# Optimization experiments

Measured on AMD Instinct MI355X. Metric: run time of the kernel, lower is better.

## Reference

```python
import jax, jax.numpy as jnp
import numpy as np

N = 100000   # nodes
F = 128      # feature dim (== numEdges ctor arg)
H = 64       # hidden_dim
E = 1600000  # edges (avg degree 16)


def setup_inputs() -> dict:
    key = jax.random.key(0)
    ks = jax.random.split(key, 8)
    x = jax.random.normal(ks[0], (N, F), dtype=jnp.float32)
    edge_index = jax.random.randint(ks[1], (2, E), 0, N)
    sF = 1.0 / np.sqrt(F)
    sH = 1.0 / np.sqrt(H)
    conv_W = jax.random.normal(ks[2], (F, F), dtype=jnp.float32) * sF  # GCNConv linear weight
    conv_b = jnp.zeros((F,), dtype=jnp.float32)
    w1 = jax.random.normal(ks[3], (H, F), dtype=jnp.float32) * sF
    b1 = jnp.zeros((H,), dtype=jnp.float32)
    w2 = jax.random.normal(ks[4], (H, H), dtype=jnp.float32) * sH
    b2 = jnp.zeros((H,), dtype=jnp.float32)
    w3 = jax.random.normal(ks[5], (1, H), dtype=jnp.float32) * sH
    b3 = jnp.zeros((1,), dtype=jnp.float32)
    return dict(x=x, edge_index=edge_index, conv_W=conv_W, conv_b=conv_b,
                w1=w1, b1=b1, w2=w2, b2=b2, w3=w3, b3=b3)


def reference(x, edge_index, conv_W, conv_b, w1, b1, w2, b2, w3, b3):
    n = x.shape[0]
    # --- GCNConv: D^{-1/2}(A+I)D^{-1/2} X W + b ---
    xw = x @ conv_W.T                                   # [N, F]
    loops = jnp.arange(n)
    src = jnp.concatenate([edge_index[0], loops])       # add self-loops
    dst = jnp.concatenate([edge_index[1], loops])
    deg = jax.ops.segment_sum(jnp.ones(src.shape[0], xw.dtype), dst, num_segments=n)
    dinv = jnp.where(deg > 0, jax.lax.rsqrt(deg), 0.0)
    norm = dinv[src] * dinv[dst]                        # [E+N]
    h = jax.ops.segment_sum(xw[src] * norm[:, None], dst, num_segments=n) + conv_b  # [N, F]
    # --- MedianAggregation (index=None -> single segment, 'lower' interpolation) ---
    med = jnp.sort(h, axis=0)[(n - 1) // 2][None, :]    # [1, F]
    # --- tanh MLP ---
    a = jnp.tanh(med @ w1.T + b1)
    a = jnp.tanh(a @ w2.T + b2)
    return a @ w3.T + b3                                # [1, 1]
```

## Files before the change

kernel.cpp:

```cpp
#include <hip/hip_runtime.h>
#include <math.h>


#define CAP    24576
#define CCAP   96
#define DSTR   32
#define OVCAP  4096
#define SPCAP  2048
#define BCAP   4608
#define NBKMAX 400
#define CH     4096

typedef __attribute__((ext_vector_type(8))) short short8;
typedef __attribute__((ext_vector_type(4))) float f32x4;
typedef __attribute__((ext_vector_type(8))) _Float16 half8;
typedef __attribute__((ext_vector_type(2))) _Float16 half2v;

__device__ __forceinline__ unsigned ordKey(float x) {
    unsigned u = __float_as_uint(x);
    return (u & 0x80000000u) ? ~u : (u | 0x80000000u);
}
__device__ __forceinline__ float keyToFloat(unsigned k) {
    unsigned bits = (k & 0x80000000u) ? (k & 0x7FFFFFFFu) : ~k;
    return __uint_as_float(bits);
}
__device__ __forceinline__ unsigned short f2bf(float f) {
    unsigned u = __float_as_uint(f);
    return (unsigned short)((u + 0x7FFFu + ((u >> 16) & 1u)) >> 16);
}

__global__ void k_init(int* __restrict__ cursor, int* __restrict__ below,
                       int* __restrict__ candCnt, int* __restrict__ ovCnt,
                       const float* __restrict__ W, short* __restrict__ Whi,
                       short* __restrict__ Wlo, int nbk) {
    if (blockIdx.x == 1) {
        for (int idx = threadIdx.x; idx < 16384; idx += 256) {
            int j = idx & 7, lane = (idx >> 3) & 63;
            int t = (idx >> 9) & 7, s = idx >> 12;
            int row = t * 16 + (lane & 15);
            int k = s * 32 + (lane >> 4) * 8 + j;
            float w = W[row * 128 + k];
            unsigned short hb = f2bf(w);
            float hf = __uint_as_float((unsigned)hb << 16);
            Whi[idx] = (short)hb;
            Wlo[idx] = (short)f2bf(w - hf);
        }
        return;
    }
    int t = threadIdx.x;
    for (int i = t; i < nbk; i += 256) cursor[i] = 0;
    if (t < 128) { below[t] = 0; candCnt[t] = 0; }
    if (t == 0) { ovCnt[0] = 0; ovCnt[1] = 0; }
}

__global__ __launch_bounds__(256) void k_binGemm(
        const float* __restrict__ x, const short* __restrict__ Whi,
        const short* __restrict__ Wlo, _Float16* __restrict__ xw, int n, int GB,
        const int* __restrict__ src, const int* __restrict__ dst, int E,
        int* __restrict__ cursor, int2* __restrict__ binned,
        int* __restrict__ ovCnt, int2* __restrict__ ovBuf, int nbk) {
    __shared__ char smem[39168];
    const int t = threadIdx.x;
    if ((int)blockIdx.x < GB) {
        float* trn = (float*)smem;
        const int lane = t & 63, wv = t >> 6;
        const int quad = lane >> 4, m = lane & 15;
        const int rowBase = blockIdx.x * 64 + wv * 16;
        const int r = rowBase + m;
        const int rl = r < n ? r : (n - 1);
        f32x4 acc[8];
        #pragma unroll
        for (int q = 0; q < 8; q++) acc[q] = (f32x4){0.f, 0.f, 0.f, 0.f};
        #pragma unroll
        for (int s = 0; s < 4; s++) {
            const float* xp = x + (size_t)rl * 128 + s * 32 + quad * 8;
            float4 p0 = *(const float4*)xp;
            float4 p1 = *(const float4*)(xp + 4);
            float f[8] = {p0.x, p0.y, p0.z, p0.w, p1.x, p1.y, p1.z, p1.w};
            short8 ah, al;
            #pragma unroll
            for (int j = 0; j < 8; j++) {
                unsigned short hb = f2bf(f[j]);
                float hf = __uint_as_float((unsigned)hb << 16);
                ah[j] = (short)hb;
                al[j] = (short)f2bf(f[j] - hf);
            }
            #pragma unroll
            for (int q = 0; q < 8; q++) {
                short8 bh = *(const short8*)(Whi + (((s * 8 + q) * 64 + lane) << 3));
                short8 bl = *(const short8*)(Wlo + (((s * 8 + q) * 64 + lane) << 3));
                acc[q] = __builtin_amdgcn_mfma_f32_16x16x32_bf16(ah, bh, acc[q], 0, 0, 0);
                acc[q] = __builtin_amdgcn_mfma_f32_16x16x32_bf16(al, bh, acc[q], 0, 0, 0);
                acc[q] = __builtin_amdgcn_mfma_f32_16x16x32_bf16(ah, bl, acc[q], 0, 0, 0);
            }
        }
        float* tw = trn + wv * (16 * 132);
        #pragma unroll
        for (int q = 0; q < 8; q++)
            #pragma unroll
            for (int e = 0; e < 4; e++)
                tw[(quad * 4 + e) * 132 + q * 16 + m] = acc[q][e];
        #pragma unroll
        for (int i = 0; i < 4; i++) {
            int row = i * 4 + (lane >> 4);
            int c8 = lane & 15;
            const float* tp = tw + row * 132 + c8 * 8;
            float4 p0 = *(const float4*)tp;
            float4 p1 = *(const float4*)(tp + 4);
            half8 o;
            o[0] = (_Float16)p0.x; o[1] = (_Float16)p0.y;
            o[2] = (_Float16)p0.z; o[3] = (_Float16)p0.w;
            o[4] = (_Float16)p1.x; o[5] = (_Float16)p1.y;
            o[6] = (_Float16)p1.z; o[7] = (_Float16)p1.w;
            int grow = rowBase + row;
            if (grow < n) *(half8*)(xw + (size_t)grow * 128 + c8 * 8) = o;
        }
    } else {
        int2* stage = (int2*)smem;
        int* hist  = (int*)(smem + 32768);
        int* gbase = hist + NBKMAX;
        int* hist2 = gbase + NBKMAX;
        int* sbase = hist2 + NBKMAX;
        const int e0 = ((int)blockIdx.x - GB) * CH;
        const int len = min(CH, E - e0);
        for (int i = t; i < nbk; i += 256) { hist[i] = 0; hist2[i] = 0; }
        __syncthreads();
        for (int k = t; k < len; k += 256) {
            int s = src[e0 + k], d = dst[e0 + k];
            stage[k] = make_int2(s, d);
            atomicAdd(&hist[d >> 8], 1);
        }
        __syncthreads();
        for (int i = t; i < nbk; i += 256) {
            int c = hist[i];
            if (c) {
                int g = atomicAdd(&cursor[i], c);
                if (g + c <= BCAP) gbase[i] = g;
                else {
                    gbase[i] = -1;
                    sbase[i] = atomicAdd(ovCnt, c);
                }
            }
        }
        __syncthreads();
        for (int k = t; k < len; k += 256) {
            int2 e = stage[k];
            int b = e.y >> 8;
            int p = atomicAdd(&hist2[b], 1);
            int g = gbase[b];
            if (g >= 0) binned[(size_t)b * BCAP + g + p] = e;
            else {
                int o = sbase[b] + p;
                if (o < OVCAP) ovBuf[o] = make_int2(e.y, e.x);
            }
        }
    }
}

__global__ __launch_bounds__(256) void k_build(int2* __restrict__ binned,
                                               const int* __restrict__ cursor,
                                               float* __restrict__ dinv,
                                               unsigned char* __restrict__ deg8,
                                               int* __restrict__ ovCnt,
                                               int2* __restrict__ ovBuf,
                                               int* __restrict__ spillNodes, int n) {
    __shared__ int ladj[256 * DSTR];
    __shared__ int lcnt[256];
    const int b = blockIdx.x, t = threadIdx.x;
    const int cnt = min(cursor[b], BCAP);
    const size_t e0 = (size_t)b * BCAP;
    lcnt[t] = 0;
    __syncthreads();
    for (int k = t; k < cnt; k += 256) {
        int2 e = binned[e0 + k];
        int li = e.y & 255;
        int pos = atomicAdd(&lcnt[li], 1);
        if (pos < DSTR) ladj[li * DSTR + pos] = e.x;
        else {
            int o = atomicAdd(ovCnt, 1);
            if (o < OVCAP) ovBuf[o] = make_int2(e.y, e.x);
        }
    }
    __syncthreads();
    int4* adjOut = (int4*)((int*)binned + e0 * 2);
    const int4* lsrc4 = (const int4*)ladj;
    for (int i = t; i < 2048; i += 256) adjOut[i] = lsrc4[i];
    int node = b * 256 + t;
    if (node < n) {
        int deg = lcnt[t];
        dinv[node] = (float)(1.0 / sqrt((double)(deg + 1)));
        deg8[node] = (unsigned char)(deg < 255 ? deg : 255);
        if (deg > DSTR) {
            int p = atomicAdd(ovCnt + 1, 1);
            if (p < SPCAP) spillNodes[p] = node;
        }
    }
}

__global__ __launch_bounds__(256) void k_aggS(const _Float16* __restrict__ xw,
                                              const unsigned char* __restrict__ deg8,
                                              const int* __restrict__ adjAll,
                                              const float* __restrict__ dinv,
                                              const float* __restrict__ conv_b,
                                              float* __restrict__ hS, int n, int ns) {
    const int si = blockIdx.x * 4 + (threadIdx.x >> 6);
    if (si >= ns) return;
    const int d = si << 5;
    const int lane = threadIdx.x & 63;
    const int l32 = lane & 31;
    int degT = deg8[d];
    const int degB = degT < DSTR ? degT : DSTR;
    const float dd = dinv[d];
    const int* adjRow = adjAll + (size_t)(d >> 8) * (BCAP * 2) + (d & 255) * DSTR;
    int aj = adjRow[l32];
    bool ev = (lane < 32) && (l32 < degB);
    int ajs = ev ? aj : 0;
    float dv = ev ? dinv[ajs] : 0.f;
    const half2v* xwv = (const half2v*)xw;
    half2v a = xwv[(size_t)d * 64 + lane];
    float ax = dd * dd * (float)a.x, ay = dd * dd * (float)a.y;
    int j = 0;
    for (; j + 8 <= degB; j += 8) {
        int s[8];
        float w[8];
        #pragma unroll
        for (int q = 0; q < 8; q++) {
            s[q] = __shfl(ajs, j + q, 64);
            w[q] = dd * __shfl(dv, j + q, 64);
        }
        #pragma unroll
        for (int q = 0; q < 8; q++) {
            half2v v = xwv[(size_t)s[q] * 64 + lane];
            ax += w[q] * (float)v.x;
            ay += w[q] * (float)v.y;
        }
    }
    if (j < degB) {
        int s[8];
        float w[8];
        #pragma unroll
        for (int q = 0; q < 8; q++) {
            int idx = j + q;
            bool ok = idx < degB;
            int lsrc = ok ? idx : 0;
            int sv = __shfl(ajs, lsrc, 64);
            float wv = dd * __shfl(dv, lsrc, 64);
            s[q] = ok ? sv : 0;
            w[q] = ok ? wv : 0.f;
        }
        #pragma unroll
        for (int q = 0; q < 8; q++) {
            half2v v = xwv[(size_t)s[q] * 64 + lane];
            ax += w[q] * (float)v.x;
            ay += w[q] * (float)v.y;
        }
    }
    float2 cb = ((const float2*)conv_b)[lane];
    float2 o;
    o.x = ax + cb.x;
    o.y = ay + cb.y;
    ((float2*)hS)[(size_t)si * 64 + lane] = o;
}

__global__ __launch_bounds__(256) void k_sample(const float* __restrict__ hS, int n,
                                                unsigned* __restrict__ Lkey,
                                                unsigned* __restrict__ Ukey) {
    __shared__ int hist[2048];
    __shared__ int wsum[4];
    const int c = blockIdx.x, t = threadIdx.x;
    for (int i = t; i < 2048; i += 256) hist[i] = 0;
    __syncthreads();
    const int ns = (n + 31) >> 5;
    for (int i = t; i < ns; i += 256) {
        float v = hS[(size_t)i * 128 + c];
        atomicAdd(&hist[ordKey(v) >> 21], 1);
    }
    __syncthreads();
    int ps = 0;
    #pragma unroll
    for (int b = 0; b < 8; b++) ps += hist[t * 8 + b];
    const int lane = t & 63, wv = t >> 6;
    int sc = ps;
    #pragma unroll
    for (int off = 1; off < 64; off <<= 1) {
        int y = __shfl_up(sc, off, 64);
        if (lane >= off) sc += y;
    }
    if (lane == 63) wsum[wv] = sc;
    __syncthreads();
    int wbase = 0;
    for (int ww = 0; ww < wv; ww++) wbase += wsum[ww];
    const int excl = wbase + sc - ps;
    const int sMid = (ns - 1) >> 1;
    const int delta = (int)(4.0f * sqrtf((float)ns)) + 1;
    int sLo = sMid - delta; if (sLo < 0) sLo = 0;
    int sHi = sMid + delta; if (sHi > ns - 1) sHi = ns - 1;
    if (sLo >= excl && sLo < excl + ps) {
        int rem = sLo - excl, b = t * 8;
        for (;; b++) { int cc = hist[b]; if (rem < cc) break; rem -= cc; }
        Lkey[c] = (unsigned)b << 21;
    }
    if (sHi >= excl && sHi < excl + ps) {
        int rem = sHi - excl, b = t * 8;
        for (;; b++) { int cc = hist[b]; if (rem < cc) break; rem -= cc; }
        Ukey[c] = (((unsigned)(b + 1)) << 21) - 1u;
    }
}

__global__ __launch_bounds__(256) void k_aggH(const _Float16* __restrict__ xw,
                                              const unsigned char* __restrict__ deg8,
                                              const int* __restrict__ adjAll,
                                              const float* __restrict__ dinv,
                                              const float* __restrict__ conv_b,
                                              _Float16* __restrict__ h, int n) {
    const int d = blockIdx.x * 4 + (threadIdx.x >> 6);
    if (d >= n) return;
    const int lane = threadIdx.x & 63;
    const int l32 = lane & 31;
    int degT = deg8[d];
    const int degB = degT < DSTR ? degT : DSTR;
    const float dd = dinv[d];
    const int* adjRow = adjAll + (size_t)(d >> 8) * (BCAP * 2) + (d & 255) * DSTR;
    int aj = adjRow[l32];
    bool ev = (lane < 32) && (l32 < degB);
    int ajs = ev ? aj : 0;
    float dv = ev ? dinv[ajs] : 0.f;
    const half2v* xwv = (const half2v*)xw;
    half2v a = xwv[(size_t)d * 64 + lane];
    float ax = dd * dd * (float)a.x, ay = dd * dd * (float)a.y;
    int j = 0;
    for (; j + 8 <= degB; j += 8) {
        int s[8];
        float w[8];
        #pragma unroll
        for (int q = 0; q < 8; q++) {
            s[q] = __shfl(ajs, j + q, 64);
            w[q] = dd * __shfl(dv, j + q, 64);
        }
        #pragma unroll
        for (int q = 0; q < 8; q++) {
            half2v v = xwv[(size_t)s[q] * 64 + lane];
            ax += w[q] * (float)v.x;
            ay += w[q] * (float)v.y;
        }
    }
    if (j < degB) {
        int s[8];
        float w[8];
        #pragma unroll
        for (int q = 0; q < 8; q++) {
            int idx = j + q;
            bool ok = idx < degB;
            int lsrc = ok ? idx : 0;
            int sv = __shfl(ajs, lsrc, 64);
            float wv = dd * __shfl(dv, lsrc, 64);
            s[q] = ok ? sv : 0;
            w[q] = ok ? wv : 0.f;
        }
        #pragma unroll
        for (int q = 0; q < 8; q++) {
            half2v v = xwv[(size_t)s[q] * 64 + lane];
            ax += w[q] * (float)v.x;
            ay += w[q] * (float)v.y;
        }
    }
    float2 cb = ((const float2*)conv_b)[lane];
    half2v o;
    o.x = (_Float16)(ax + cb.x);
    o.y = (_Float16)(ay + cb.y);
    ((half2v*)h)[(size_t)d * 64 + lane] = o;
}

__global__ void k_spillFix(const _Float16* __restrict__ xw,
                           const int* __restrict__ spillNodes,
                           const int* __restrict__ adjAll,
                           const float* __restrict__ dinv,
                           const float* __restrict__ conv_b,
                           const int2* __restrict__ ovBuf,
                           const int* __restrict__ ovCnt,
                           _Float16* __restrict__ h) {
    int m = ovCnt[0];  if (m > OVCAP) m = OVCAP;
    int sp = ovCnt[1]; if (sp > SPCAP) sp = SPCAP;
    const int t = threadIdx.x;
    for (int i = blockIdx.x; i < sp; i += gridDim.x) {
        const int d = spillNodes[i];
        const float dd = dinv[d];
        float acc = dd * dd * (float)xw[(size_t)d * 128 + t];
        const int* adjRow = adjAll + (size_t)(d >> 8) * (BCAP * 2) + (d & 255) * DSTR;
        for (int j = 0; j < DSTR; j++) {
            int a = adjRow[j];
            acc += dd * dinv[a] * (float)xw[(size_t)a * 128 + t];
        }
        for (int k = 0; k < m; k++) {
            int2 e = ovBuf[k];
            if (e.x == d)
                acc += dd * dinv[e.y] * (float)xw[(size_t)e.y * 128 + t];
        }
        h[(size_t)d * 128 + t] = (_Float16)(acc + conv_b[t]);
    }
}

__global__ __launch_bounds__(256) void k_classify(const _Float16* __restrict__ h,
                                                  int total8,
                                                  const unsigned* __restrict__ Lkey,
                                                  const unsigned* __restrict__ Ukey,
                                                  int* __restrict__ below,
                                                  int* __restrict__ candCnt,
                                                  float* __restrict__ cand) {
    __shared__ float buf[128 * CCAP];
    __shared__ int cN[128], cB[128];
    const int t = threadIdx.x;
    for (int i = t; i < 128; i += 256) { cN[i] = 0; cB[i] = 0; }
    __syncthreads();
    const int stride = gridDim.x * blockDim.x;
    const int i0 = blockIdx.x * blockDim.x + t;
    const int jb = (i0 << 3) & 127;
    unsigned L[8], U[8];
    #pragma unroll
    for (int k = 0; k < 8; k++) { L[k] = Lkey[jb + k]; U[k] = Ukey[jb + k]; }
    int b[8] = {0, 0, 0, 0, 0, 0, 0, 0};
    const half8* hv = (const half8*)h;
    for (int i = i0; i < total8; i += stride) {
        half8 v = hv[i];
        #pragma unroll
        for (int k = 0; k < 8; k++) {
            float f = (float)v[k];
            unsigned u = ordKey(f);
            if (u < L[k]) b[k]++;
            else if (u <= U[k]) {
                int p = atomicAdd(&cN[jb + k], 1);
                if (p < CCAP) buf[(jb + k) * CCAP + p] = f;
                else {
                    int g = atomicAdd(&candCnt[jb + k], 1);
                    if (g < CAP) cand[(size_t)(jb + k) * CAP + g] = f;
                }
            }
        }
    }
    #pragma unroll
    for (int k = 0; k < 8; k++)
        if (b[k]) atomicAdd(&cB[jb + k], b[k]);
    __syncthreads();
    if (t < 128) {
        if (cB[t]) atomicAdd(&below[t], cB[t]);
        int nn = cN[t] < CCAP ? cN[t] : CCAP;
        if (nn) {
            int base = atomicAdd(&candCnt[t], nn);
            for (int k2 = 0; k2 < nn && base + k2 < CAP; k2++)
                cand[(size_t)t * CAP + base + k2] = buf[t * CCAP + k2];
        }
    }
}

__global__ __launch_bounds__(256) void k_final(const float* __restrict__ cand,
                                               const int* __restrict__ candCnt,
                                               const int* __restrict__ below, int n,
                                               float* __restrict__ med) {
    __shared__ int hist[2048];
    __shared__ unsigned sPre;
    __shared__ int sRank;
    const int c = blockIdx.x, t = threadIdx.x;
    int cnt = candCnt[c]; if (cnt > CAP) cnt = CAP;
    const float* cp = cand + (size_t)c * CAP;
    if (t == 0) {
        int r = (n - 1) / 2 - below[c];
        if (r < 0) r = 0;
        if (r >= cnt) r = cnt - 1;
        sRank = r;
        sPre = 0u;
    }
    __syncthreads();
    #pragma unroll
    for (int round = 0; round < 3; round++) {
        const int nb = (round == 2) ? 1024 : 2048;
        for (int i = t; i < nb; i += 256) hist[i] = 0;
        __syncthreads();
        for (int i = t; i < cnt; i += 256) {
            unsigned u = ordKey(cp[i]);
            bool ok;
            int bin;
            if (round == 0)      { ok = true;                      bin = u >> 21; }
            else if (round == 1) { ok = (u >> 21) == (sPre >> 21); bin = (u >> 10) & 2047; }
            else                 { ok = (u >> 10) == (sPre >> 10); bin = u & 1023; }
            if (ok) atomicAdd(&hist[bin], 1);
        }
        __syncthreads();
        if (t < 64) {
            const int per = nb >> 6;
            int ps = 0;
            for (int b = t * per; b < t * per + per; b++) ps += hist[b];
            int sc = ps;
            #pragma unroll
            for (int off = 1; off < 64; off <<= 1) {
                int y = __shfl_up(sc, off, 64);
                if (t >= off) sc += y;
            }
            int excl = sc - ps;
            int r = sRank;
            if (excl <= r && r < sc) {
                int b = t * per, rem = r - excl;
                for (;; b++) {
                    int cc = hist[b];
                    if (rem < cc) break;
                    rem -= cc;
                }
                if (round == 0)      sPre = (unsigned)b << 21;
                else if (round == 1) sPre |= (unsigned)b << 10;
                else                 sPre |= (unsigned)b;
                sRank = rem;
            }
        }
        __syncthreads();
    }
    if (t == 0) med[c] = keyToFloat(sPre);
}

__global__ void k_mlp(const float* __restrict__ med,
                      const float* __restrict__ w1, const float* __restrict__ b1,
                      const float* __restrict__ w2, const float* __restrict__ b2,
                      const float* __restrict__ w3, const float* __restrict__ b3,
                      float* __restrict__ out) {
    __shared__ float m[128], a1[64], a2[64];
    int t = threadIdx.x;
    if (t < 128) m[t] = med[t];
    __syncthreads();
    if (t < 64) {
        float acc = b1[t];
        for (int f = 0; f < 128; f++) acc += m[f] * w1[t * 128 + f];
        a1[t] = tanhf(acc);
    }
    __syncthreads();
    if (t < 64) {
        float acc = b2[t];
        for (int f = 0; f < 64; f++) acc += a1[f] * w2[t * 64 + f];
        a2[t] = tanhf(acc);
    }
    __syncthreads();
    if (t == 0) {
        float acc = b3[0];
        for (int f = 0; f < 64; f++) acc += a2[f] * w3[f];
        out[0] = acc;
    }
}

extern "C" void kernel_launch(void* const* d_in, const int* in_sizes, int n_in,
                              void* d_out, int out_size, void* d_ws, size_t ws_size,
                              hipStream_t stream) {
    const float* x      = (const float*)d_in[0];
    const int*   ei     = (const int*)d_in[1];
    const float* conv_W = (const float*)d_in[2];
    const float* conv_b = (const float*)d_in[3];
    const float* w1 = (const float*)d_in[4];
    const float* b1 = (const float*)d_in[5];
    const float* w2 = (const float*)d_in[6];
    const float* b2 = (const float*)d_in[7];
    const float* w3 = (const float*)d_in[8];
    const float* b3 = (const float*)d_in[9];

    const int N = in_sizes[0] / 128;
    const int E = in_sizes[1] / 2;
    const int* src = ei;
    const int* dst = ei + E;
    const int NBK = (N + 255) / 256;
    const int NS  = (N + 31) >> 5;

    char* p = (char*)d_ws;
    auto alloc = [&](size_t bytes) -> char* {
        char* q = p;
        p += (bytes + 255) & ~(size_t)255;
        return q;
    };
    _Float16* xw  = (_Float16*)alloc((size_t)N * 128 * 2);
    _Float16* h   = (_Float16*)alloc((size_t)N * 128 * 2);
    int2*  binned = (int2*)alloc((size_t)NBK * BCAP * 8);
    float* cand   = (float*)alloc((size_t)128 * CAP * 4);
    float* hS     = (float*)alloc((size_t)NS * 128 * 4);
    float* dinv   = (float*)alloc((size_t)N * 4);
    unsigned char* deg8 = (unsigned char*)alloc((size_t)N);
    int*   cursor = (int*)alloc((size_t)NBK * 4);
    short* Whi    = (short*)alloc(16384 * 2);
    short* Wlo    = (short*)alloc(16384 * 2);
    int2*  ovBuf  = (int2*)alloc((size_t)OVCAP * 8);
    int*   ovCnt  = (int*)alloc(256);
    int*   spillNodes = (int*)alloc((size_t)SPCAP * 4);
    unsigned* Lkey = (unsigned*)alloc(128 * 4);
    unsigned* Ukey = (unsigned*)alloc(128 * 4);
    int*   below   = (int*)alloc(128 * 4);
    int*   candCnt = (int*)alloc(128 * 4);
    float* med     = (float*)alloc(128 * 4);

    const int GB   = (N + 63) / 64;
    const int BINB = (E + CH - 1) / CH;

    k_init<<<2, 256, 0, stream>>>(cursor, below, candCnt, ovCnt, conv_W, Whi, Wlo, NBK);
    k_binGemm<<<GB + BINB, 256, 0, stream>>>(x, Whi, Wlo, xw, N, GB,
                                             src, dst, E, cursor, binned,
                                             ovCnt, ovBuf, NBK);
    k_build<<<NBK, 256, 0, stream>>>(binned, cursor, dinv, deg8, ovCnt, ovBuf,
                                     spillNodes, N);
    k_aggS<<<(NS + 3) / 4, 256, 0, stream>>>(xw, deg8, (const int*)binned, dinv,
                                             conv_b, hS, N, NS);
    k_sample<<<128, 256, 0, stream>>>(hS, N, Lkey, Ukey);
    k_aggH<<<(N + 3) / 4, 256, 0, stream>>>(xw, deg8, (const int*)binned, dinv,
                                            conv_b, h, N);
    k_spillFix<<<16, 128, 0, stream>>>(xw, spillNodes, (const int*)binned, dinv,
                                       conv_b, ovBuf, ovCnt, h);
    k_classify<<<1024, 256, 0, stream>>>(h, N * 16, Lkey, Ukey, below, candCnt, cand);
    k_final<<<128, 256, 0, stream>>>(cand, candCnt, below, N, med);
    k_mlp<<<1, 128, 0, stream>>>(med, w1, b1, w2, b2, w3, b3, (float*)d_out);
}
```

Baseline: 326.5 us.

## Sample median bounds from final fp16 h, drop separate sampled aggregation kernel

```diff
diff --git a/kernel.cpp b/kernel.cpp
--- a/kernel.cpp
+++ b/kernel.cpp
@@ -19,10 +19,6 @@
 __device__ __forceinline__ unsigned ordKey(float x) {
     unsigned u = __float_as_uint(x);
     return (u & 0x80000000u) ? ~u : (u | 0x80000000u);
-}
-__device__ __forceinline__ float keyToFloat(unsigned k) {
-    unsigned bits = (k & 0x80000000u) ? (k & 0x7FFFFFFFu) : ~k;
-    return __uint_as_float(bits);
 }
 __device__ __forceinline__ unsigned short f2bf(float f) {
     unsigned u = __float_as_uint(f);
@@ -157,7 +153,7 @@
     }
 }
 
-__global__ __launch_bounds__(256) void k_build(int2* __restrict__ binned,
+__global__ __launch_bounds__(512) void k_build(int2* __restrict__ binned,
                                                const int* __restrict__ cursor,
                                                float* __restrict__ dinv,
                                                unsigned char* __restrict__ deg8,
@@ -169,9 +165,9 @@
     const int b = blockIdx.x, t = threadIdx.x;
     const int cnt = min(cursor[b], BCAP);
     const size_t e0 = (size_t)b * BCAP;
-    lcnt[t] = 0;
-    __syncthreads();
-    for (int k = t; k < cnt; k += 256) {
+    if (t < 256) lcnt[t] = 0;
+    __syncthreads();
+    for (int k = t; k < cnt; k += 512) {
         int2 e = binned[e0 + k];
         int li = e.y & 255;
         int pos = atomicAdd(&lcnt[li], 1);
@@ -184,126 +180,18 @@
     __syncthreads();
     int4* adjOut = (int4*)((int*)binned + e0 * 2);
     const int4* lsrc4 = (const int4*)ladj;
-    for (int i = t; i < 2048; i += 256) adjOut[i] = lsrc4[i];
-    int node = b * 256 + t;
-    if (node < n) {
-        int deg = lcnt[t];
-        dinv[node] = (float)(1.0 / sqrt((double)(deg + 1)));
-        deg8[node] = (unsigned char)(deg < 255 ? deg : 255);
-        if (deg > DSTR) {
-            int p = atomicAdd(ovCnt + 1, 1);
-            if (p < SPCAP) spillNodes[p] = node;
-        }
-    }
-}
-
-__global__ __launch_bounds__(256) void k_aggS(const _Float16* __restrict__ xw,
-                                              const unsigned char* __restrict__ deg8,
-                                              const int* __restrict__ adjAll,
-                                              const float* __restrict__ dinv,
-                                              const float* __restrict__ conv_b,
-                                              float* __restrict__ hS, int n, int ns) {
-    const int si = blockIdx.x * 4 + (threadIdx.x >> 6);
-    if (si >= ns) return;
-    const int d = si << 5;
-    const int lane = threadIdx.x & 63;
-    const int l32 = lane & 31;
-    int degT = deg8[d];
-    const int degB = degT < DSTR ? degT : DSTR;
-    const float dd = dinv[d];
-    const int* adjRow = adjAll + (size_t)(d >> 8) * (BCAP * 2) + (d & 255) * DSTR;
-    int aj = adjRow[l32];
-    bool ev = (lane < 32) && (l32 < degB);
-    int ajs = ev ? aj : 0;
-    float dv = ev ? dinv[ajs] : 0.f;
-    const half2v* xwv = (const half2v*)xw;
-    half2v a = xwv[(size_t)d * 64 + lane];
-    float ax = dd * dd * (float)a.x, ay = dd * dd * (float)a.y;
-    int j = 0;
-    for (; j + 8 <= degB; j += 8) {
-        int s[8];
-        float w[8];
-        #pragma unroll
-        for (int q = 0; q < 8; q++) {
-            s[q] = __shfl(ajs, j + q, 64);
-            w[q] = dd * __shfl(dv, j + q, 64);
-        }
-        #pragma unroll
-        for (int q = 0; q < 8; q++) {
-            half2v v = xwv[(size_t)s[q] * 64 + lane];
-            ax += w[q] * (float)v.x;
-            ay += w[q] * (float)v.y;
-        }
-    }
-    if (j < degB) {
-        int s[8];
-        float w[8];
-        #pragma unroll
-        for (int q = 0; q < 8; q++) {
-            int idx = j + q;
-            bool ok = idx < degB;
-            int lsrc = ok ? idx : 0;
-            int sv = __shfl(ajs, lsrc, 64);
-            float wv = dd * __shfl(dv, lsrc, 64);
-            s[q] = ok ? sv : 0;
-            w[q] = ok ? wv : 0.f;
-        }
-        #pragma unroll
-        for (int q = 0; q < 8; q++) {
-            half2v v = xwv[(size_t)s[q] * 64 + lane];
-            ax += w[q] * (float)v.x;
-            ay += w[q] * (float)v.y;
-        }
-    }
-    float2 cb = ((const float2*)conv_b)[lane];
-    float2 o;
-    o.x = ax + cb.x;
-    o.y = ay + cb.y;
-    ((float2*)hS)[(size_t)si * 64 + lane] = o;
-}
-
-__global__ __launch_bounds__(256) void k_sample(const float* __restrict__ hS, int n,
-                                                unsigned* __restrict__ Lkey,
-                                                unsigned* __restrict__ Ukey) {
-    __shared__ int hist[2048];
-    __shared__ int wsum[4];
-    const int c = blockIdx.x, t = threadIdx.x;
-    for (int i = t; i < 2048; i += 256) hist[i] = 0;
-    __syncthreads();
-    const int ns = (n + 31) >> 5;
-    for (int i = t; i < ns; i += 256) {
-        float v = hS[(size_t)i * 128 + c];
-        atomicAdd(&hist[ordKey(v) >> 21], 1);
-    }
-    __syncthreads();
-    int ps = 0;
-    #pragma unroll
-    for (int b = 0; b < 8; b++) ps += hist[t * 8 + b];
-    const int lane = t & 63, wv = t >> 6;
-    int sc = ps;
-    #pragma unroll
-    for (int off = 1; off < 64; off <<= 1) {
-        int y = __shfl_up(sc, off, 64);
-        if (lane >= off) sc += y;
-    }
-    if (lane == 63) wsum[wv] = sc;
-    __syncthreads();
-    int wbase = 0;
-    for (int ww = 0; ww < wv; ww++) wbase += wsum[ww];
-    const int excl = wbase + sc - ps;
-    const int sMid = (ns - 1) >> 1;
-    const int delta = (int)(4.0f * sqrtf((float)ns)) + 1;
-    int sLo = sMid - delta; if (sLo < 0) sLo = 0;
-    int sHi = sMid + delta; if (sHi > ns - 1) sHi = ns - 1;
-    if (sLo >= excl && sLo < excl + ps) {
-        int rem = sLo - excl, b = t * 8;
-        for (;; b++) { int cc = hist[b]; if (rem < cc) break; rem -= cc; }
-        Lkey[c] = (unsigned)b << 21;
-    }
-    if (sHi >= excl && sHi < excl + ps) {
-        int rem = sHi - excl, b = t * 8;
-        for (;; b++) { int cc = hist[b]; if (rem < cc) break; rem -= cc; }
-        Ukey[c] = (((unsigned)(b + 1)) << 21) - 1u;
+    for (int i = t; i < 2048; i += 512) adjOut[i] = lsrc4[i];
+    if (t < 256) {
+        int node = b * 256 + t;
+        if (node < n) {
+            int deg = lcnt[t];
+            dinv[node] = (float)(1.0 / sqrt((double)(deg + 1)));
+            deg8[node] = (unsigned char)(deg < 255 ? deg : 255);
+            if (deg > DSTR) {
+                int p = atomicAdd(ovCnt + 1, 1);
+                if (p < SPCAP) spillNodes[p] = node;
+            }
+        }
     }
 }
 
@@ -400,14 +288,59 @@
     }
 }
 
+__global__ __launch_bounds__(256) void k_sample(const _Float16* __restrict__ h, int n,
+                                                unsigned* __restrict__ Lkey,
+                                                unsigned* __restrict__ Ukey) {
+    __shared__ int hist[2048];
+    __shared__ int wsum[4];
+    const int c = blockIdx.x, t = threadIdx.x;
+    for (int i = t; i < 2048; i += 256) hist[i] = 0;
+    __syncthreads();
+    const int ns = (n + 31) >> 5;
+    for (int i = t; i < ns; i += 256) {
+        float v = (float)h[(size_t)(i << 5) * 128 + c];
+        atomicAdd(&hist[ordKey(v) >> 21], 1);
+    }
+    __syncthreads();
+    int ps = 0;
+    #pragma unroll
+    for (int b = 0; b < 8; b++) ps += hist[t * 8 + b];
+    const int lane = t & 63, wv = t >> 6;
+    int sc = ps;
+    #pragma unroll
+    for (int off = 1; off < 64; off <<= 1) {
+        int y = __shfl_up(sc, off, 64);
+        if (lane >= off) sc += y;
+    }
+    if (lane == 63) wsum[wv] = sc;
+    __syncthreads();
+    int wbase = 0;
+    for (int ww = 0; ww < wv; ww++) wbase += wsum[ww];
+    const int excl = wbase + sc - ps;
+    const int sMid = (ns - 1) >> 1;
+    const int delta = (int)(4.0f * sqrtf((float)ns)) + 1;
+    int sLo = sMid - delta; if (sLo < 0) sLo = 0;
+    int sHi = sMid + delta; if (sHi > ns - 1) sHi = ns - 1;
+    if (sLo >= excl && sLo < excl + ps) {
+        int rem = sLo - excl, b = t * 8;
+        for (;; b++) { int cc = hist[b]; if (rem < cc) break; rem -= cc; }
+        Lkey[c] = (unsigned)b << 21;
+    }
+    if (sHi >= excl && sHi < excl + ps) {
+        int rem = sHi - excl, b = t * 8;
+        for (;; b++) { int cc = hist[b]; if (rem < cc) break; rem -= cc; }
+        Ukey[c] = (((unsigned)(b + 1)) << 21) - 1u;
+    }
+}
+
 __global__ __launch_bounds__(256) void k_classify(const _Float16* __restrict__ h,
                                                   int total8,
                                                   const unsigned* __restrict__ Lkey,
                                                   const unsigned* __restrict__ Ukey,
                                                   int* __restrict__ below,
                                                   int* __restrict__ candCnt,
-                                                  float* __restrict__ cand) {
-    __shared__ float buf[128 * CCAP];
+                                                  _Float16* __restrict__ cand) {
+    __shared__ _Float16 buf[128 * CCAP];
     __shared__ int cN[128], cB[128];
     const int t = threadIdx.x;
     for (int i = t; i < 128; i += 256) { cN[i] = 0; cB[i] = 0; }
@@ -429,10 +362,10 @@
             if (u < L[k]) b[k]++;
             else if (u <= U[k]) {
                 int p = atomicAdd(&cN[jb + k], 1);
-                if (p < CCAP) buf[(jb + k) * CCAP + p] = f;
+                if (p < CCAP) buf[(jb + k) * CCAP + p] = v[k];
                 else {
                     int g = atomicAdd(&candCnt[jb + k], 1);
-                    if (g < CAP) cand[(size_t)(jb + k) * CAP + g] = f;
+                    if (g < CAP) cand[(size_t)(jb + k) * CAP + g] = v[k];
                 }
             }
         }
@@ -452,67 +385,77 @@
     }
 }
 
-__global__ __launch_bounds__(256) void k_final(const float* __restrict__ cand,
+__global__ __launch_bounds__(256) void k_final(const _Float16* __restrict__ cand,
                                                const int* __restrict__ candCnt,
                                                const int* __restrict__ below, int n,
                                                float* __restrict__ med) {
     __shared__ int hist[2048];
-    __shared__ unsigned sPre;
+    __shared__ int sSel;
     __shared__ int sRank;
     const int c = blockIdx.x, t = threadIdx.x;
     int cnt = candCnt[c]; if (cnt > CAP) cnt = CAP;
-    const float* cp = cand + (size_t)c * CAP;
+    const unsigned short* cp = (const unsigned short*)(cand + (size_t)c * CAP);
     if (t == 0) {
         int r = (n - 1) / 2 - below[c];
         if (r < 0) r = 0;
         if (r >= cnt) r = cnt - 1;
         sRank = r;
-        sPre = 0u;
-    }
-    __syncthreads();
-    #pragma unroll
-    for (int round = 0; round < 3; round++) {
-        const int nb = (round == 2) ? 1024 : 2048;
-        for (int i = t; i < nb; i += 256) hist[i] = 0;
-        __syncthreads();
-        for (int i = t; i < cnt; i += 256) {
-            unsigned u = ordKey(cp[i]);
-            bool ok;
-            int bin;
-            if (round == 0)      { ok = true;                      bin = u >> 21; }
-            else if (round == 1) { ok = (u >> 21) == (sPre >> 21); bin = (u >> 10) & 2047; }
-            else                 { ok = (u >> 10) == (sPre >> 10); bin = u & 1023; }
-            if (ok) atomicAdd(&hist[bin], 1);
-        }
-        __syncthreads();
-        if (t < 64) {
-            const int per = nb >> 6;
-            int ps = 0;
-            for (int b = t * per; b < t * per + per; b++) ps += hist[b];
-            int sc = ps;
-            #pragma unroll
-            for (int off = 1; off < 64; off <<= 1) {
-                int y = __shfl_up(sc, off, 64);
-                if (t >= off) sc += y;
-            }
-            int excl = sc - ps;
-            int r = sRank;
-            if (excl <= r && r < sc) {
-                int b = t * per, rem = r - excl;
-                for (;; b++) {
-                    int cc = hist[b];
-                    if (rem < cc) break;
-                    rem -= cc;
-                }
-                if (round == 0)      sPre = (unsigned)b << 21;
-                else if (round == 1) sPre |= (unsigned)b << 10;
-                else                 sPre |= (unsigned)b;
-                sRank = rem;
-            }
-        }
-        __syncthreads();
-    }
-    if (t == 0) med[c] = keyToFloat(sPre);
+        sSel = 0;
+    }
+    for (int i = t; i < 2048; i += 256) hist[i] = 0;
+    __syncthreads();
+    for (int i = t; i < cnt; i += 256) {
+        unsigned ub = cp[i];
+        unsigned k = (ub & 0x8000u) ? (~ub & 0xFFFFu) : (ub | 0x8000u);
+        atomicAdd(&hist[k >> 5], 1);
+    }
+    __syncthreads();
+    if (t < 64) {
+        int ps = 0;
+        for (int b = t * 32; b < t * 32 + 32; b++) ps += hist[b];
+        int sc = ps;
+        #pragma unroll
+        for (int off = 1; off < 64; off <<= 1) {
+            int y = __shfl_up(sc, off, 64);
+            if (t >= off) sc += y;
+        }
+        int excl = sc - ps;
+        int r = sRank;
+        if (excl <= r && r < sc) {
+            int b = t * 32, rem = r - excl;
+            for (;; b++) {
+                int cc = hist[b];
+                if (rem < cc) break;
+                rem -= cc;
+            }
+            sSel = b;
+            sRank = rem;
+        }
+    }
+    __syncthreads();
+    if (t < 32) hist[t] = 0;
+    __syncthreads();
+    const int sel = sSel;
+    for (int i = t; i < cnt; i += 256) {
+        unsigned ub = cp[i];
+        unsigned k = (ub & 0x8000u) ? (~ub & 0xFFFFu) : (ub | 0x8000u);
+        if ((int)(k >> 5) == sel) atomicAdd(&hist[k & 31], 1);
+    }
+    __syncthreads();
+    if (t == 0) {
+        int rem = sRank, b = 0;
+        for (;; b++) {
+            int cc = hist[b];
+            if (rem < cc) break;
+            rem -= cc;
+        }
+        unsigned key16 = ((unsigned)sel << 5) | (unsigned)b;
+        unsigned short bits = (key16 & 0x8000u) ? (unsigned short)(key16 & 0x7FFFu)
+                                                : (unsigned short)(~key16 & 0xFFFFu);
+        _Float16 hv;
+        *(unsigned short*)&hv = bits;
+        med[c] = (float)hv;
+    }
 }
 
 __global__ void k_mlp(const float* __restrict__ med,
@@ -562,7 +505,6 @@
     const int* src = ei;
     const int* dst = ei + E;
     const int NBK = (N + 255) / 256;
-    const int NS  = (N + 31) >> 5;
 
     char* p = (char*)d_ws;
     auto alloc = [&](size_t bytes) -> char* {
@@ -573,8 +515,7 @@
     _Float16* xw  = (_Float16*)alloc((size_t)N * 128 * 2);
     _Float16* h   = (_Float16*)alloc((size_t)N * 128 * 2);
     int2*  binned = (int2*)alloc((size_t)NBK * BCAP * 8);
-    float* cand   = (float*)alloc((size_t)128 * CAP * 4);
-    float* hS     = (float*)alloc((size_t)NS * 128 * 4);
+    _Float16* cand = (_Float16*)alloc((size_t)128 * CAP * 2);
     float* dinv   = (float*)alloc((size_t)N * 4);
     unsigned char* deg8 = (unsigned char*)alloc((size_t)N);
     int*   cursor = (int*)alloc((size_t)NBK * 4);
@@ -596,16 +537,14 @@
     k_binGemm<<<GB + BINB, 256, 0, stream>>>(x, Whi, Wlo, xw, N, GB,
                                              src, dst, E, cursor, binned,
                                              ovCnt, ovBuf, NBK);
-    k_build<<<NBK, 256, 0, stream>>>(binned, cursor, dinv, deg8, ovCnt, ovBuf,
+    k_build<<<NBK, 512, 0, stream>>>(binned, cursor, dinv, deg8, ovCnt, ovBuf,
                                      spillNodes, N);
-    k_aggS<<<(NS + 3) / 4, 256, 0, stream>>>(xw, deg8, (const int*)binned, dinv,
-                                             conv_b, hS, N, NS);
-    k_sample<<<128, 256, 0, stream>>>(hS, N, Lkey, Ukey);
     k_aggH<<<(N + 3) / 4, 256, 0, stream>>>(xw, deg8, (const int*)binned, dinv,
                                             conv_b, h, N);
     k_spillFix<<<16, 128, 0, stream>>>(xw, spillNodes, (const int*)binned, dinv,
                                        conv_b, ovBuf, ovCnt, h);
-    k_classify<<<1024, 256, 0, stream>>>(h, N * 16, Lkey, Ukey, below, candCnt, cand);
+    k_sample<<<128, 256, 0, stream>>>(h, N, Lkey, Ukey);
+    k_classify<<<2048, 256, 0, stream>>>(h, N * 16, Lkey, Ukey, below, candCnt, cand);
     k_final<<<128, 256, 0, stream>>>(cand, candCnt, below, N, med);
     k_mlp<<<1, 128, 0, stream>>>(med, w1, b1, w2, b2, w3, b3, (float*)d_out);
 }
```

Measured after the change: 316.4 us. -3.1%, faster.
